# Kernel tuning notes

Measured on AMD Instinct MI355X. Metric: run time of the kernel, lower is better.

Reference implementation:

```python
import jax, jax.numpy as jnp
import numpy as np

EPS = 1e-5
THRESH = 0.05
NUM_THINGS = 3
D = 256
EGO_PC_RANGE = np.array([-51.2, -51.2, -5.0, 51.2, 51.2, 3.0], np.float32)


def _inverse_sigmoid(x):
    x = jnp.clip(x, 0.0, 1.0)
    return jnp.log(jnp.maximum(x, EPS) / jnp.maximum(1.0 - x, EPS))


def setup_inputs() -> dict:
    key = jax.random.key(0)
    ks = jax.random.split(key, 16)
    L, B, Qo, Qv = 6, 1, 8192, 8192
    # class logits uniform in [0,1) -> sigmoid >= 0.5 > threshold, so all queries pass (deterministic shapes)
    other_outputs_classes = jax.random.uniform(ks[0], (L, B, Qo, NUM_THINGS), jnp.float32)
    other_outputs_coords = jax.random.uniform(ks[1], (L, B, Qo, 4), jnp.float32)
    other_query = jax.random.normal(ks[2], (B, Qo, D), jnp.float32)
    other_query_pos = jax.random.normal(ks[3], (B, Qo, D), jnp.float32)
    other_reference = jax.random.normal(ks[4], (B, Qo, 4), jnp.float32)
    veh_outputs_classes = jax.random.normal(ks[5], (L, B, Qv, NUM_THINGS), jnp.float32)
    veh_outputs_coords = jax.random.uniform(ks[6], (L, B, Qv, 4), jnp.float32)
    veh_query = jax.random.normal(ks[7], (B, Qv, D), jnp.float32)
    veh_query_pos = jax.random.normal(ks[8], (B, Qv, D), jnp.float32)
    veh_reference = jax.random.normal(ks[9], (B, Qv, 4), jnp.float32)
    # rigid ego->other transform (rotation about z + translation), invertible by construction
    th = 0.3
    rt = np.eye(4, dtype=np.float32)
    rt[0, 0] = np.cos(th); rt[0, 1] = -np.sin(th)
    rt[1, 0] = np.sin(th); rt[1, 1] = np.cos(th)
    rt[0, 3] = 12.0; rt[1, 3] = -5.0; rt[2, 3] = 0.3
    ego2other_rt = jnp.asarray(rt)[None]  # [1,4,4]
    other_agent_pc_range = jnp.asarray(EGO_PC_RANGE)
    xav = float(np.sqrt(2.0 / (D + 9 + D)))
    Wa = jax.random.normal(ks[10], (D + 9, D), jnp.float32) * xav
    ba = jax.random.normal(ks[11], (D,), jnp.float32) * 0.01
    Wp = jax.random.normal(ks[12], (D + 9, D), jnp.float32) * xav
    bp = jax.random.normal(ks[13], (D,), jnp.float32) * 0.01
    return dict(other_outputs_classes=other_outputs_classes, other_outputs_coords=other_outputs_coords,
                other_query=other_query, other_query_pos=other_query_pos, other_reference=other_reference,
                veh_outputs_classes=veh_outputs_classes, veh_outputs_coords=veh_outputs_coords,
                veh_query=veh_query, veh_query_pos=veh_query_pos, veh_reference=veh_reference,
                ego2other_rt=ego2other_rt, other_agent_pc_range=other_agent_pc_range,
                Wa=Wa, ba=ba, Wp=Wp, bp=bp)


def reference(other_outputs_classes, other_outputs_coords, other_query, other_query_pos, other_reference,
              veh_outputs_classes, veh_outputs_coords, veh_query, veh_query_pos, veh_reference,
              ego2other_rt, other_agent_pc_range, Wa, ba, Wp, bp):
    calib = jnp.linalg.inv(ego2other_rt[0].T)  # other -> ego, [4,4]
    # filter_other_lanes (eager: concrete inputs, data-dependent selection like torch.where)
    cls = jax.nn.sigmoid(other_outputs_classes[-1])
    bbox_index = jnp.where(cls.reshape(-1) > THRESH)[0] // NUM_THINGS
    ooc_cls = other_outputs_classes[:, :, bbox_index]      # [L,B,N,3]
    ooc = other_outputs_coords[:, :, bbox_index]           # [L,B,N,4]
    oq = other_query[:, bbox_index]                        # [B,N,D]
    oqp = other_query_pos[:, bbox_index]
    oref = other_reference[:, bbox_index]                  # [B,N,4]
    lo, hi = other_agent_pc_range[:3], other_agent_pc_range[3:]
    elo = jnp.asarray(EGO_PC_RANGE[:3]); ehi = jnp.asarray(EGO_PC_RANGE[3:])
    # --- reference points: inverse_sigmoid space, z logit = 0 ---
    p = jax.nn.sigmoid(jnp.concatenate([oref[..., :2], jnp.zeros_like(oref[..., :1])], -1))
    p = p * (hi - lo) + lo                                 # other lidar coords
    h = jnp.concatenate([p, jnp.ones_like(p[..., :1])], -1)
    p = jnp.einsum('ij,bnj->bni', calib, h)[..., :3]       # ego lidar coords
    p = _inverse_sigmoid((p - elo) / (ehi - elo))
    oref = jnp.concatenate([p[..., :2], oref[..., 2:]], -1)
    # --- bbox centers: already sigmoided, z norm = 0 ---
    b = jnp.concatenate([ooc[..., :2], jnp.zeros_like(ooc[..., :1])], -1)
    b = b * (hi - lo) + lo
    hb = jnp.concatenate([b, jnp.ones_like(b[..., :1])], -1)
    b = jnp.einsum('ij,lbnj->lbni', calib, hb)[..., :3]
    b = (b - elo) / (ehi - elo)
    ooc = jnp.concatenate([b[..., :2], ooc[..., 2:]], -1)
    # --- cross-agent query alignment: concat flattened 3x3 rotation, small Linear ---
    r9 = jnp.broadcast_to(calib[:3, :3].reshape(9), oq.shape[:2] + (9,))
    oq = jnp.concatenate([oq, r9], -1) @ Wa + ba
    oqp = jnp.concatenate([oqp, r9], -1) @ Wp + bp
    return (jnp.concatenate([veh_outputs_classes, ooc_cls], axis=2),
            jnp.concatenate([veh_outputs_coords, ooc], axis=2),
            jnp.concatenate([veh_query, oq], axis=1),
            jnp.concatenate([veh_query_pos, oqp], axis=1),
            jnp.concatenate([veh_reference, oref], axis=1))
```

## Files before the change

kernel.cpp:

```cpp
#include <hip/hip_runtime.h>
#include <stdint.h>

typedef float f32x4 __attribute__((ext_vector_type(4)));
typedef __bf16 bf16x8 __attribute__((ext_vector_type(8)));

namespace {
constexpr int L = 6, Qo = 8192, Qv = 8192, NT = 3, D = 256;
constexpr int ROWS = Qv + 3 * Qo;
constexpr int OUT0 = 0;
constexpr int OUT1 = L * ROWS * NT;
constexpr int OUT2 = OUT1 + L * ROWS * 4;
constexpr int OUT3 = OUT2 + ROWS * D;
constexpr int OUT4 = OUT3 + ROWS * D;
constexpr float ELO0 = -51.2f, ELO1 = -51.2f, EHI0 = 51.2f, EHI1 = 51.2f;
constexpr int NB_GEMM = 512;
constexpr int NB_STREAM = 1536;
constexpr int NB_TOT = NB_GEMM + NB_STREAM;
constexpr int LDSA = 16384;
constexpr int LDSBIAS = LDSA + 32768;
constexpr int LDSCAL = LDSBIAS + 128;
constexpr int R_COPY = 2 * Qv * D / 4;
constexpr int R_OUT1 = R_COPY + L * ROWS;
constexpr int R_OUT4 = R_OUT1 + ROWS;
constexpr int R_TOT  = R_OUT4 + L * ROWS * NT / 4;
}

__device__ __forceinline__ float sigmoidf(float x) { return 1.f / (1.f + __expf(-x)); }
__device__ __forceinline__ float invsig(float v) {
    float x = fminf(fmaxf(v, 0.f), 1.f);
    return __logf(fmaxf(x, 1e-5f) / fmaxf(1.f - x, 1e-5f));
}

__device__ void inv4x4_T(const float* __restrict__ rt, float* __restrict__ C) {
    float m[16], inv[16];
    for (int i = 0; i < 4; i++)
        for (int j = 0; j < 4; j++) m[i * 4 + j] = rt[j * 4 + i];
    inv[0]  =  m[5]*m[10]*m[15] - m[5]*m[11]*m[14] - m[9]*m[6]*m[15] + m[9]*m[7]*m[14] + m[13]*m[6]*m[11] - m[13]*m[7]*m[10];
    inv[4]  = -m[4]*m[10]*m[15] + m[4]*m[11]*m[14] + m[8]*m[6]*m[15] - m[8]*m[7]*m[14] - m[12]*m[6]*m[11] + m[12]*m[7]*m[10];
    inv[8]  =  m[4]*m[9]*m[15]  - m[4]*m[11]*m[13] - m[8]*m[5]*m[15] + m[8]*m[7]*m[13] + m[12]*m[5]*m[11] - m[12]*m[7]*m[9];
    inv[12] = -m[4]*m[9]*m[14]  + m[4]*m[10]*m[13] + m[8]*m[5]*m[14] - m[8]*m[6]*m[13] - m[12]*m[5]*m[10] + m[12]*m[6]*m[9];
    inv[1]  = -m[1]*m[10]*m[15] + m[1]*m[11]*m[14] + m[9]*m[2]*m[15] - m[9]*m[3]*m[14] - m[13]*m[2]*m[11] + m[13]*m[3]*m[10];
    inv[5]  =  m[0]*m[10]*m[15] - m[0]*m[11]*m[14] - m[8]*m[2]*m[15] + m[8]*m[3]*m[14] + m[12]*m[2]*m[11] - m[12]*m[3]*m[10];
    inv[9]  = -m[0]*m[9]*m[15]  + m[0]*m[11]*m[13] + m[8]*m[1]*m[15] - m[8]*m[3]*m[13] - m[12]*m[1]*m[11] + m[12]*m[3]*m[9];
    inv[13] =  m[0]*m[9]*m[14]  - m[0]*m[10]*m[13] - m[8]*m[1]*m[14] + m[8]*m[2]*m[13] + m[12]*m[1]*m[10] - m[12]*m[2]*m[9];
    inv[2]  =  m[1]*m[6]*m[15]  - m[1]*m[7]*m[14]  - m[5]*m[2]*m[15] + m[5]*m[3]*m[14] + m[13]*m[2]*m[7]  - m[13]*m[3]*m[6];
    inv[6]  = -m[0]*m[6]*m[15]  + m[0]*m[7]*m[14]  + m[4]*m[2]*m[15] - m[4]*m[3]*m[14] - m[12]*m[2]*m[7]  + m[12]*m[3]*m[6];
    inv[10] =  m[0]*m[5]*m[15]  - m[0]*m[7]*m[13]  - m[4]*m[1]*m[15] + m[4]*m[3]*m[13] + m[12]*m[1]*m[7]  - m[12]*m[3]*m[5];
    inv[14] = -m[0]*m[5]*m[14]  + m[0]*m[6]*m[13]  + m[4]*m[1]*m[14] - m[4]*m[2]*m[13] - m[12]*m[1]*m[6]  + m[12]*m[2]*m[5];
    inv[3]  = -m[1]*m[6]*m[11]  + m[1]*m[7]*m[10]  + m[5]*m[2]*m[11] - m[5]*m[3]*m[10] - m[9]*m[2]*m[7]   + m[9]*m[3]*m[6];
    inv[7]  =  m[0]*m[6]*m[11]  - m[0]*m[7]*m[10]  - m[4]*m[2]*m[11] + m[4]*m[3]*m[10] + m[8]*m[2]*m[7]   - m[8]*m[3]*m[6];
    inv[11] = -m[0]*m[5]*m[11]  + m[0]*m[7]*m[9]   + m[4]*m[1]*m[11] - m[4]*m[3]*m[9]  - m[8]*m[1]*m[7]   + m[8]*m[3]*m[5];
    inv[15] =  m[0]*m[5]*m[10]  - m[0]*m[6]*m[9]   - m[4]*m[1]*m[10] + m[4]*m[2]*m[9]  + m[8]*m[1]*m[6]   - m[8]*m[2]*m[5];
    float det = m[0]*inv[0] + m[1]*inv[4] + m[2]*inv[8] + m[3]*inv[12];
    det = 1.0f / det;
    for (int i = 0; i < 16; i++) C[i] = inv[i] * det;
}

__global__ __launch_bounds__(256) void fused(
    const float* __restrict__ ocls, const float* __restrict__ ocoord,
    const float* __restrict__ oq, const float* __restrict__ oqp,
    const float* __restrict__ oref, const float* __restrict__ vcls,
    const float* __restrict__ vcoord, const float* __restrict__ vq,
    const float* __restrict__ vqp, const float* __restrict__ vref,
    const float* __restrict__ rt, const float* __restrict__ pcr,
    const float* __restrict__ Wa, const float* __restrict__ ba,
    const float* __restrict__ Wp, const float* __restrict__ bp,
    float* __restrict__ out) {
    __shared__ __attribute__((aligned(16))) char lds[49344];
    float* ldsBias  = (float*)&lds[LDSBIAS];
    float* ldsCalib = (float*)&lds[LDSCAL];
    const int b = blockIdx.x;
    const int t = threadIdx.x;

    if (b < NB_GEMM) {
        const int r = b & 7, ny = (b >> 3) & 7, s = b >> 6;
        const int u = s * 8 + r, which = u >> 5, mg = u & 31;
        const float* Asrc = which ? oqp : oq;
        const float* Wsrc = which ? Wp : Wa;
        const float* bv   = which ? bp : ba;
        const size_t obase = which ? (size_t)OUT3 : (size_t)OUT2;
        const int n0 = ny * 32;
        if (t == 0) inv4x4_T(rt, ldsCalib);
        f32x4 pre[16];
        {
            const float* Abase = Asrc + (size_t)(mg * 4) * 64 * D;
            #pragma unroll
            for (int i = 0; i < 8; ++i) {
                int flat = i * 256 + t;
                int row = flat >> 5, cu8 = flat & 31;
                const float* src = Abase + (size_t)row * D + cu8 * 8;
                pre[2 * i]     = *(const f32x4*)src;
                pre[2 * i + 1] = *(const f32x4*)(src + 4);
            }
        }
        {
            int kloc = t >> 3;
            int n4 = (t & 7) * 4;
            #pragma unroll
            for (int pass = 0; pass < 8; ++pass) {
                int k = pass * 32 + kloc;
                f32x4 v = *(const f32x4*)&Wsrc[(size_t)k * D + n0 + n4];
                #pragma unroll
                for (int i = 0; i < 4; ++i) {
                    int n = n4 + i;
                    *(__bf16*)&lds[n * 512 + ((2 * k) ^ ((n & 7) << 4))] = (__bf16)v[i];
                }
            }
        }
        __syncthreads();
        if (t < 32) {
            float sum = bv[n0 + t];
            #pragma unroll
            for (int m2 = 0; m2 < 9; m2++)
                sum += ldsCalib[(m2 / 3) * 4 + (m2 % 3)] * Wsrc[(size_t)(D + m2) * D + n0 + t];
            ldsBias[t] = sum;
        }
        __syncthreads();
        const int lane = t & 63, wave = t >> 6, lrow = lane & 15, grp = lane >> 4;
        for (int mi = 0; mi < 4; ++mi) {
            #pragma unroll
            for (int i = 0; i < 8; ++i) {
                int flat = i * 256 + t;
                int row = flat >> 5;
                int cu8 = flat & 31;
                f32x4 a0 = pre[2 * i], a1 = pre[2 * i + 1];
                bf16x8 w = {(__bf16)a0.x, (__bf16)a0.y, (__bf16)a0.z, (__bf16)a0.w,
                            (__bf16)a1.x, (__bf16)a1.y, (__bf16)a1.z, (__bf16)a1.w};
                *(bf16x8*)&lds[LDSA + row * 512 + ((cu8 * 16) ^ ((row & 7) << 4))] = w;
            }
            __syncthreads();
            if (mi < 3) {
                const float* Abase = Asrc + (size_t)(mg * 4 + mi + 1) * 64 * D;
                #pragma unroll
                for (int i = 0; i < 8; ++i) {
                    int flat = i * 256 + t;
                    int row = flat >> 5, cu8 = flat & 31;
                    const float* src = Abase + (size_t)row * D + cu8 * 8;
                    pre[2 * i]     = *(const f32x4*)src;
                    pre[2 * i + 1] = *(const f32x4*)(src + 4);
                }
            }
            const int arow = wave * 16 + lrow;
            const int abase = LDSA + arow * 512;
            const int aswz = (lrow & 7) << 4;
            f32x4 acc[2] = {f32x4{0, 0, 0, 0}, f32x4{0, 0, 0, 0}};
            #pragma unroll
            for (int ks = 0; ks < 8; ++ks) {
                int kb = ks * 64 + grp * 16;
                bf16x8 af = *(const bf16x8*)&lds[abase + (kb ^ aswz)];
                #pragma unroll
                for (int nt = 0; nt < 2; ++nt) {
                    int c = nt * 16 + lrow;
                    bf16x8 w = *(const bf16x8*)&lds[c * 512 + (kb ^ ((c & 7) << 4))];
                    acc[nt] = __builtin_amdgcn_mfma_f32_16x16x32_bf16(w, af, acc[nt], 0, 0, 0);
                }
            }
            __syncthreads();
            const int am = (mg * 4 + mi) * 64 + arow;
            size_t rbase = obase + (size_t)(Qv + 3 * am) * D + n0;
            #pragma unroll
            for (int nt = 0; nt < 2; ++nt) {
                f32x4 bz = *(const f32x4*)&ldsBias[nt * 16 + grp * 4];
                f32x4 v = acc[nt] + bz;
                float* p = out + rbase + nt * 16 + grp * 4;
                *(f32x4*)p = v;
                *(f32x4*)(p + D) = v;
                *(f32x4*)(p + 2 * D) = v;
            }
        }
        return;
    }

    if (t == 0) inv4x4_T(rt, ldsCalib);
    __syncthreads();
    const float c00 = ldsCalib[0], c01 = ldsCalib[1], c02 = ldsCalib[2], c03 = ldsCalib[3];
    const float c10 = ldsCalib[4], c11 = ldsCalib[5], c12 = ldsCalib[6], c13 = ldsCalib[7];
    const float lo0 = pcr[0], lo1 = pcr[1], lo2 = pcr[2];
    const float hi0 = pcr[3], hi1 = pcr[4], hi2 = pcr[5];
    const int stride = NB_STREAM * 256;
    for (int c = (b - NB_GEMM) * 256 + t; c < R_TOT; c += stride) {
        if (c < R_COPY) {
            const int HALF = Qv * D / 4;
            const float* src = (c < HALF) ? vq : vqp;
            size_t ob = (c < HALF) ? (size_t)OUT2 : (size_t)OUT3;
            int jj = (c < HALF) ? c : c - HALF;
            *(f32x4*)&out[ob + (size_t)jj * 4] = *(const f32x4*)&src[(size_t)jj * 4];
        } else if (c < R_OUT1) {
            int tid = c - R_COPY;
            unsigned l = (unsigned)tid >> 15, rr = (unsigned)tid & 32767u;
            f32x4 o;
            if (rr < (unsigned)Qv) {
                o = *(const f32x4*)&vcoord[((size_t)l * Qv + rr) * 4];
            } else {
                unsigned q = (rr - Qv) / 3u;
                f32x4 s = *(const f32x4*)&ocoord[((size_t)l * Qo + q) * 4];
                float bx = s.x * (hi0 - lo0) + lo0;
                float by = s.y * (hi1 - lo1) + lo1;
                float bz = lo2;
                float px = c00 * bx + c01 * by + c02 * bz + c03;
                float py = c10 * bx + c11 * by + c12 * bz + c13;
                o.x = (px - ELO0) / (EHI0 - ELO0);
                o.y = (py - ELO1) / (EHI1 - ELO1);
                o.z = s.z; o.w = s.w;
            }
            *(f32x4*)&out[OUT1 + (size_t)tid * 4] = o;
        } else if (c < R_OUT4) {
            unsigned rr = (unsigned)(c - R_OUT1);
            f32x4 o;
            if (rr < (unsigned)Qv) {
                o = *(const f32x4*)&vref[(size_t)rr * 4];
            } else {
                unsigned q = (rr - Qv) / 3u;
                f32x4 s = *(const f32x4*)&oref[(size_t)q * 4];
                float bx = sigmoidf(s.x) * (hi0 - lo0) + lo0;
                float by = sigmoidf(s.y) * (hi1 - lo1) + lo1;
                float bz = 0.5f * (hi2 - lo2) + lo2;
                float px = c00 * bx + c01 * by + c02 * bz + c03;
                float py = c10 * bx + c11 * by + c12 * bz + c13;
                o.x = invsig((px - ELO0) / (EHI0 - ELO0));
                o.y = invsig((py - ELO1) / (EHI1 - ELO1));
                o.z = s.z; o.w = s.w;
            }
            *(f32x4*)&out[OUT4 + (size_t)rr * 4] = o;
        } else {
            int e0 = (c - R_OUT4) * 4;
            f32x4 o;
            #pragma unroll
            for (int i = 0; i < 4; ++i) {
                unsigned e = (unsigned)(e0 + i);
                unsigned l = e / (unsigned)(ROWS * NT);
                unsigned rem = e - l * (ROWS * NT);
                unsigned rr = rem / 3u;
                float v;
                if (rr < (unsigned)Qv) v = vcls[l * (Qv * NT) + rem];
                else {
                    unsigned cc = rem - rr * 3u;
                    unsigned q = (rr - Qv) / 3u;
                    v = ocls[l * (Qo * NT) + q * 3u + cc];
                }
                o[i] = v;
            }
            *(f32x4*)&out[OUT0 + (size_t)e0] = o;
        }
    }
}

extern "C" void kernel_launch(void* const* d_in, const int* in_sizes, int n_in,
                              void* d_out, int out_size, void* d_ws, size_t ws_size,
                              hipStream_t stream) {
    const float* ocls   = (const float*)d_in[0];
    const float* ocoord = (const float*)d_in[1];
    const float* oq     = (const float*)d_in[2];
    const float* oqp    = (const float*)d_in[3];
    const float* oref   = (const float*)d_in[4];
    const float* vcls   = (const float*)d_in[5];
    const float* vcoord = (const float*)d_in[6];
    const float* vq     = (const float*)d_in[7];
    const float* vqp    = (const float*)d_in[8];
    const float* vref   = (const float*)d_in[9];
    const float* rt     = (const float*)d_in[10];
    const float* pcr    = (const float*)d_in[11];
    const float* Wa     = (const float*)d_in[12];
    const float* ba     = (const float*)d_in[13];
    const float* Wp     = (const float*)d_in[14];
    const float* bp     = (const float*)d_in[15];
    float* out = (float*)d_out;

    hipLaunchKernelGGL(fused, dim3(NB_TOT), dim3(256), 0, stream,
                       ocls, ocoord, oq, oqp, oref, vcls, vcoord, vq, vqp, vref,
                       rt, pcr, Wa, ba, Wp, bp, out);
}
```

Before: 26.68 us.

## Shrink LDS footprint by splitting A tile into K halves to raise occupancy

Cuts the shared-memory buffer from about 49KB to 32KB by staging the A tile in two K-halves of 256 bytes per row, reusing the A region for the bias, and computing the calibration inverse in registers. The lower LDS use plus a launch_bounds hint of 4 blocks per CU aims for more resident blocks, so memory streaming and GEMM work overlap better. In exchange, each 64-row tile now needs two extra barriers, and the min-blocks hint may push register pressure on the 16-vector prefetch array.

```diff
diff --git a/kernel.cpp b/kernel.cpp
--- a/kernel.cpp
+++ b/kernel.cpp
@@ -16,9 +16,8 @@
 constexpr int NB_GEMM = 512;
 constexpr int NB_STREAM = 1536;
 constexpr int NB_TOT = NB_GEMM + NB_STREAM;
+constexpr int LDSW = 0;
 constexpr int LDSA = 16384;
-constexpr int LDSBIAS = LDSA + 32768;
-constexpr int LDSCAL = LDSBIAS + 128;
 constexpr int R_COPY = 2 * Qv * D / 4;
 constexpr int R_OUT1 = R_COPY + L * ROWS;
 constexpr int R_OUT4 = R_OUT1 + ROWS;
@@ -31,9 +30,11 @@
     return __logf(fmaxf(x, 1e-5f) / fmaxf(1.f - x, 1e-5f));
 }
 
-__device__ void inv4x4_T(const float* __restrict__ rt, float* __restrict__ C) {
+__device__ __forceinline__ void inv4x4_T(const float* __restrict__ rt, float* C) {
     float m[16], inv[16];
+    #pragma unroll
     for (int i = 0; i < 4; i++)
+        #pragma unroll
         for (int j = 0; j < 4; j++) m[i * 4 + j] = rt[j * 4 + i];
     inv[0]  =  m[5]*m[10]*m[15] - m[5]*m[11]*m[14] - m[9]*m[6]*m[15] + m[9]*m[7]*m[14] + m[13]*m[6]*m[11] - m[13]*m[7]*m[10];
     inv[4]  = -m[4]*m[10]*m[15] + m[4]*m[11]*m[14] + m[8]*m[6]*m[15] - m[8]*m[7]*m[14] - m[12]*m[6]*m[11] + m[12]*m[7]*m[10];
@@ -53,10 +54,11 @@
     inv[15] =  m[0]*m[5]*m[10]  - m[0]*m[6]*m[9]   - m[4]*m[1]*m[10] + m[4]*m[2]*m[9]  + m[8]*m[1]*m[6]   - m[8]*m[2]*m[5];
     float det = m[0]*inv[0] + m[1]*inv[4] + m[2]*inv[8] + m[3]*inv[12];
     det = 1.0f / det;
+    #pragma unroll
     for (int i = 0; i < 16; i++) C[i] = inv[i] * det;
 }
 
-__global__ __launch_bounds__(256) void fused(
+__global__ __launch_bounds__(256, 4) void fused(
     const float* __restrict__ ocls, const float* __restrict__ ocoord,
     const float* __restrict__ oq, const float* __restrict__ oqp,
     const float* __restrict__ oref, const float* __restrict__ vcls,
@@ -66,9 +68,7 @@
     const float* __restrict__ Wa, const float* __restrict__ ba,
     const float* __restrict__ Wp, const float* __restrict__ bp,
     float* __restrict__ out) {
-    __shared__ __attribute__((aligned(16))) char lds[49344];
-    float* ldsBias  = (float*)&lds[LDSBIAS];
-    float* ldsCalib = (float*)&lds[LDSCAL];
+    __shared__ __attribute__((aligned(16))) char lds[32768];
     const int b = blockIdx.x;
     const int t = threadIdx.x;
 
@@ -80,15 +80,16 @@
         const float* bv   = which ? bp : ba;
         const size_t obase = which ? (size_t)OUT3 : (size_t)OUT2;
         const int n0 = ny * 32;
-        if (t == 0) inv4x4_T(rt, ldsCalib);
+        const int lane = t & 63, wave = t >> 6, lrow = lane & 15, grp = lane >> 4;
+
         f32x4 pre[16];
         {
             const float* Abase = Asrc + (size_t)(mg * 4) * 64 * D;
             #pragma unroll
             for (int i = 0; i < 8; ++i) {
-                int flat = i * 256 + t;
-                int row = flat >> 5, cu8 = flat & 31;
-                const float* src = Abase + (size_t)row * D + cu8 * 8;
+                int row = (i >> 1) * 16 + (t >> 4);
+                int uu = (i & 1) * 16 + (t & 15);
+                const float* src = Abase + (size_t)row * D + uu * 8;
                 pre[2 * i]     = *(const f32x4*)src;
                 pre[2 * i + 1] = *(const f32x4*)(src + 4);
             }
@@ -103,65 +104,73 @@
                 #pragma unroll
                 for (int i = 0; i < 4; ++i) {
                     int n = n4 + i;
-                    *(__bf16*)&lds[n * 512 + ((2 * k) ^ ((n & 7) << 4))] = (__bf16)v[i];
-                }
-            }
+                    *(__bf16*)&lds[LDSW + n * 512 + ((2 * k) ^ ((n & 7) << 4))] = (__bf16)v[i];
+                }
+            }
+        }
+        if (t < 32) {
+            float C[16];
+            inv4x4_T(rt, C);
+            float sum = bv[n0 + t];
+            #pragma unroll
+            for (int m2 = 0; m2 < 9; m2++)
+                sum += C[(m2 / 3) * 4 + (m2 % 3)] * Wsrc[(size_t)(D + m2) * D + n0 + t];
+            *(float*)&lds[LDSA + t * 4] = sum;
         }
         __syncthreads();
-        if (t < 32) {
-            float sum = bv[n0 + t];
-            #pragma unroll
-            for (int m2 = 0; m2 < 9; m2++)
-                sum += ldsCalib[(m2 / 3) * 4 + (m2 % 3)] * Wsrc[(size_t)(D + m2) * D + n0 + t];
-            ldsBias[t] = sum;
-        }
+        f32x4 bz[2];
+        bz[0] = *(const f32x4*)&lds[LDSA + (grp * 4) * 4];
+        bz[1] = *(const f32x4*)&lds[LDSA + (16 + grp * 4) * 4];
         __syncthreads();
-        const int lane = t & 63, wave = t >> 6, lrow = lane & 15, grp = lane >> 4;
+
+        const int arow = wave * 16 + lrow;
+        const int aswz = (arow & 7) << 4;
         for (int mi = 0; mi < 4; ++mi) {
-            #pragma unroll
-            for (int i = 0; i < 8; ++i) {
-                int flat = i * 256 + t;
-                int row = flat >> 5;
-                int cu8 = flat & 31;
-                f32x4 a0 = pre[2 * i], a1 = pre[2 * i + 1];
-                bf16x8 w = {(__bf16)a0.x, (__bf16)a0.y, (__bf16)a0.z, (__bf16)a0.w,
-                            (__bf16)a1.x, (__bf16)a1.y, (__bf16)a1.z, (__bf16)a1.w};
-                *(bf16x8*)&lds[LDSA + row * 512 + ((cu8 * 16) ^ ((row & 7) << 4))] = w;
-            }
-            __syncthreads();
-            if (mi < 3) {
-                const float* Abase = Asrc + (size_t)(mg * 4 + mi + 1) * 64 * D;
+            f32x4 acc[2] = {f32x4{0, 0, 0, 0}, f32x4{0, 0, 0, 0}};
+            #pragma unroll
+            for (int h = 0; h < 2; ++h) {
                 #pragma unroll
-                for (int i = 0; i < 8; ++i) {
-                    int flat = i * 256 + t;
-                    int row = flat >> 5, cu8 = flat & 31;
-                    const float* src = Abase + (size_t)row * D + cu8 * 8;
-                    pre[2 * i]     = *(const f32x4*)src;
-                    pre[2 * i + 1] = *(const f32x4*)(src + 4);
-                }
-            }
-            const int arow = wave * 16 + lrow;
-            const int abase = LDSA + arow * 512;
-            const int aswz = (lrow & 7) << 4;
-            f32x4 acc[2] = {f32x4{0, 0, 0, 0}, f32x4{0, 0, 0, 0}};
-            #pragma unroll
-            for (int ks = 0; ks < 8; ++ks) {
-                int kb = ks * 64 + grp * 16;
-                bf16x8 af = *(const bf16x8*)&lds[abase + (kb ^ aswz)];
+                for (int j = 0; j < 4; ++j) {
+                    int i = j * 2 + h;
+                    int row = j * 16 + (t >> 4);
+                    f32x4 a0 = pre[2 * i], a1 = pre[2 * i + 1];
+                    bf16x8 w = {(__bf16)a0.x, (__bf16)a0.y, (__bf16)a0.z, (__bf16)a0.w,
+                                (__bf16)a1.x, (__bf16)a1.y, (__bf16)a1.z, (__bf16)a1.w};
+                    *(bf16x8*)&lds[LDSA + row * 256 +
+                                   (((t & 15) * 16) ^ ((row & 7) << 4))] = w;
+                }
+                __syncthreads();
+                if (h == 1 && mi < 3) {
+                    const float* Abase = Asrc + (size_t)(mg * 4 + mi + 1) * 64 * D;
+                    #pragma unroll
+                    for (int i = 0; i < 8; ++i) {
+                        int row = (i >> 1) * 16 + (t >> 4);
+                        int uu = (i & 1) * 16 + (t & 15);
+                        const float* src = Abase + (size_t)row * D + uu * 8;
+                        pre[2 * i]     = *(const f32x4*)src;
+                        pre[2 * i + 1] = *(const f32x4*)(src + 4);
+                    }
+                }
                 #pragma unroll
-                for (int nt = 0; nt < 2; ++nt) {
-                    int c = nt * 16 + lrow;
-                    bf16x8 w = *(const bf16x8*)&lds[c * 512 + (kb ^ ((c & 7) << 4))];
-                    acc[nt] = __builtin_amdgcn_mfma_f32_16x16x32_bf16(w, af, acc[nt], 0, 0, 0);
-                }
-            }
-            __syncthreads();
+                for (int ks = 0; ks < 4; ++ks) {
+                    int kbA = ks * 64 + grp * 16;
+                    bf16x8 af = *(const bf16x8*)&lds[LDSA + arow * 256 + (kbA ^ aswz)];
+                    int kbW = h * 256 + kbA;
+                    #pragma unroll
+                    for (int nt = 0; nt < 2; ++nt) {
+                        int c = nt * 16 + lrow;
+                        bf16x8 w =
+                            *(const bf16x8*)&lds[LDSW + c * 512 + (kbW ^ ((c & 7) << 4))];
+                        acc[nt] = __builtin_amdgcn_mfma_f32_16x16x32_bf16(w, af, acc[nt], 0, 0, 0);
+                    }
+                }
+                __syncthreads();
+            }
             const int am = (mg * 4 + mi) * 64 + arow;
             size_t rbase = obase + (size_t)(Qv + 3 * am) * D + n0;
             #pragma unroll
             for (int nt = 0; nt < 2; ++nt) {
-                f32x4 bz = *(const f32x4*)&ldsBias[nt * 16 + grp * 4];
-                f32x4 v = acc[nt] + bz;
+                f32x4 v = acc[nt] + bz[nt];
                 float* p = out + rbase + nt * 16 + grp * 4;
                 *(f32x4*)p = v;
                 *(f32x4*)(p + D) = v;
@@ -171,6 +180,7 @@
         return;
     }
 
+    float* ldsCalib = (float*)lds;
     if (t == 0) inv4x4_T(rt, ldsCalib);
     __syncthreads();
     const float c00 = ldsCalib[0], c01 = ldsCalib[1], c02 = ldsCalib[2], c03 = ldsCalib[3];
```

Measured after the change: 26.30 us (median of 2 runs). Within noise of the previous version (-1.4%).
